# Optimization experiments

Hardware: AMD Instinct MI355X
Metric: run time of the kernel (lower is better)

## Reference

```python
import jax, jax.numpy as jnp
import numpy as np

N_NODES = 32768   # 32 graphs x 1024 points
B_GRAPHS = 32
RATIO = 16
C_IN = 64
HEADS = 4
NEG_SLOPE = 0.2


def setup_inputs() -> dict:
    key = jax.random.key(0)
    ks = jax.random.split(key, 8)
    H, C = HEADS, C_IN
    x = jax.random.normal(ks[0], (N_NODES, C_IN), dtype=jnp.float32)
    edge_index = jax.random.randint(ks[1], (2, 1000), 0, N_NODES)  # ignored by forward
    batch = jnp.repeat(jnp.arange(B_GRAPHS), N_NODES // B_GRAPHS)  # sorted graph ids
    xcent_base = jax.random.normal(ks[2], (RATIO, C_IN), dtype=jnp.float32)
    s = 1.0 / np.sqrt(C_IN)
    W_l = jax.random.normal(ks[3], (C_IN, H * C), dtype=jnp.float32) * s
    b_l = jnp.zeros((H * C,), dtype=jnp.float32)
    W_r = jax.random.normal(ks[4], (C_IN, H * C), dtype=jnp.float32) * s
    b_r = jnp.zeros((H * C,), dtype=jnp.float32)
    att = jax.random.normal(ks[5], (H, C), dtype=jnp.float32) * s
    bias = jnp.zeros((C,), dtype=jnp.float32)
    return {"x": x, "edge_index": edge_index, "batch": batch,
            "xcent_base": xcent_base, "W_l": W_l, "b_l": b_l,
            "W_r": W_r, "b_r": b_r, "att": att, "bias": bias,
            "ratio": RATIO, "batch_size": B_GRAPHS}


def reference(x, edge_index, batch, xcent_base, W_l, b_l, W_r, b_r, att, bias,
              ratio, batch_size):
    # GATv2Conv bipartite: (x_src, x_dst=tiled xcent_base), concat=False (mean over heads)
    H, C = att.shape
    N = x.shape[0]
    T = batch_size * ratio                       # number of target centroids
    # edge list: each source node -> all `ratio` centroids of its graph
    src = jnp.repeat(jnp.arange(N), ratio)       # [E]
    tgt = jnp.tile(jnp.arange(ratio), N) + jnp.repeat(batch, ratio) * ratio  # [E]
    x_dst = jnp.tile(xcent_base, (batch_size, 1))          # [T, C_in]
    x_l = (x @ W_l + b_l).reshape(N, H, C)                 # source transform
    x_r = (x_dst @ W_r + b_r).reshape(T, H, C)             # target transform
    z = x_l[src] + x_r[tgt]                                # [E, H, C]
    z = jnp.where(z >= 0, z, NEG_SLOPE * z)                # LeakyReLU(0.2)
    logit = jnp.einsum('ehc,hc->eh', z, att)               # [E, H]
    # segment softmax over edges sharing a target centroid
    m = jax.ops.segment_max(logit, tgt, num_segments=T)
    ex = jnp.exp(logit - m[tgt])
    den = jax.ops.segment_sum(ex, tgt, num_segments=T)
    alpha = ex / den[tgt]                                  # [E, H]
    out = jax.ops.segment_sum(x_l[src] * alpha[:, :, None], tgt, num_segments=T)
    xcent = out.mean(axis=1) + bias                        # [T, C] (concat=False)
    batchcent = jnp.repeat(jnp.arange(batch_size), ratio)  # [T]
    return xcent, batchcent
```

## Files before the change

### kernel.cpp

```cpp
#include <hip/hip_runtime.h>


typedef __attribute__((ext_vector_type(8))) short short8;
typedef __attribute__((ext_vector_type(4))) float f32x4;

#define NPG 1024
#define NT 512

static __device__ __forceinline__ unsigned short f2bf(float f) {
    unsigned int u = __float_as_uint(f);
    u += 0x7fffu + ((u >> 16) & 1u);
    return (unsigned short)(u >> 16);
}
static __device__ __forceinline__ float bf2f(unsigned short u) {
    return __uint_as_float(((unsigned int)u) << 16);
}

__global__ __launch_bounds__(256) void k0_prep(const float* __restrict__ xcb,
                                               const float* __restrict__ W_l,
                                               const float* __restrict__ W_r,
                                               const float* __restrict__ b_r,
                                               const float* __restrict__ att,
                                               float* __restrict__ xrT,
                                               float* __restrict__ xr_att6,
                                               float* __restrict__ att6,
                                               float* __restrict__ att4,
                                               unsigned short* __restrict__ wt,
                                               float* __restrict__ out) {
    int b = blockIdx.x, t = threadIdx.x;
    if (b < 16) {
        int r = b, hc = t;
        float v = b_r[hc];
#pragma unroll
        for (int k = 0; k < 64; ++k)
            v = fmaf(xcb[r * 64 + k], W_r[k * 256 + hc], v);
        xrT[hc * 16 + r] = v;
        float p = 0.6f * att[hc] * v;
        p += __shfl_xor(p, 1);  p += __shfl_xor(p, 2);
        p += __shfl_xor(p, 4);  p += __shfl_xor(p, 8);
        p += __shfl_xor(p, 16); p += __shfl_xor(p, 32);
        if ((t & 63) == 0) xr_att6[r * 4 + (t >> 6)] = p;
    } else {
        att6[t] = 0.6f * att[t];
        att4[t] = 0.4f * att[t];
        unsigned short tmp[64] __attribute__((aligned(16)));
#pragma unroll
        for (int k = 0; k < 64; ++k) tmp[k] = f2bf(W_l[k * 256 + t]);
#pragma unroll
        for (int q = 0; q < 8; ++q)
            *(short8*)(wt + t * 64 + q * 8) = *(const short8*)(tmp + q * 8);
        out[NT * 64 + t]       = (float)(t >> 4);
        out[NT * 64 + 256 + t] = (float)((256 + t) >> 4);
    }
}

__global__ __launch_bounds__(256, 2) void k1_fused(const float* __restrict__ x,
                                                   const unsigned short* __restrict__ wt,
                                                   const float* __restrict__ b_l,
                                                   const float* __restrict__ att6,
                                                   const float* __restrict__ att4,
                                                   const float* __restrict__ xrT,
                                                   const float* __restrict__ xr_att6,
                                                   unsigned short* __restrict__ ws_pvh,
                                                   float* __restrict__ ws_denp) {
    __shared__ __align__(16) unsigned char smraw[(256 + 64) * 72 * 2];
    unsigned short (*As)[72]  = (unsigned short (*)[72])smraw;
    unsigned short (*xlT)[72] = (unsigned short (*)[72])smraw;
    unsigned short (*exT)[72] = (unsigned short (*)[72])(smraw + 256 * 72 * 2);

    const int t = threadIdx.x;
    const int blk = blockIdx.x;
    const int n0 = blk * 64;

    {
        int n = t >> 2, q = (t & 3) * 16;
        const float* p = x + (size_t)(n0 + n) * 64 + q;
        float4 v0 = *(const float4*)p;
        float4 v1 = *(const float4*)(p + 4);
        float4 v2 = *(const float4*)(p + 8);
        float4 v3 = *(const float4*)(p + 12);
        unsigned short h16[16] __attribute__((aligned(16)));
        h16[0]=f2bf(v0.x); h16[1]=f2bf(v0.y); h16[2]=f2bf(v0.z); h16[3]=f2bf(v0.w);
        h16[4]=f2bf(v1.x); h16[5]=f2bf(v1.y); h16[6]=f2bf(v1.z); h16[7]=f2bf(v1.w);
        h16[8]=f2bf(v2.x); h16[9]=f2bf(v2.y); h16[10]=f2bf(v2.z); h16[11]=f2bf(v2.w);
        h16[12]=f2bf(v3.x); h16[13]=f2bf(v3.y); h16[14]=f2bf(v3.z); h16[15]=f2bf(v3.w);
        *(short8*)(&As[n][q])     = *(const short8*)h16;
        *(short8*)(&As[n][q + 8]) = *(const short8*)(h16 + 8);
    }
    __syncthreads();

    const int l = t & 63;
    const int h = __builtin_amdgcn_readfirstlane(t >> 6);
    const int lm = l & 15, lk = (l >> 4) * 8;

    short8 af[4][2], bfr[4][2];
#pragma unroll
    for (int mt = 0; mt < 4; ++mt)
#pragma unroll
        for (int ks = 0; ks < 2; ++ks)
            af[mt][ks] = *(const short8*)(&As[mt * 16 + lm][ks * 32 + lk]);
#pragma unroll
    for (int nt = 0; nt < 4; ++nt)
#pragma unroll
        for (int ks = 0; ks < 2; ++ks)
            bfr[nt][ks] = *(const short8*)(wt + (size_t)(h * 64 + nt * 16 + lm) * 64 + ks * 32 + lk);

    f32x4 acc[4][4];
#pragma unroll
    for (int mt = 0; mt < 4; ++mt)
#pragma unroll
        for (int nt = 0; nt < 4; ++nt) { f32x4 z = {0.f,0.f,0.f,0.f}; acc[mt][nt] = z; }
#pragma unroll
    for (int mt = 0; mt < 4; ++mt)
#pragma unroll
        for (int nt = 0; nt < 4; ++nt)
#pragma unroll
            for (int ks = 0; ks < 2; ++ks)
                acc[mt][nt] = __builtin_amdgcn_mfma_f32_16x16x32_bf16(
                    af[mt][ks], bfr[nt][ks], acc[mt][nt], 0, 0, 0);

    __syncthreads();

#pragma unroll
    for (int nt = 0; nt < 4; ++nt) {
        float bl = b_l[h * 64 + nt * 16 + lm];
#pragma unroll
        for (int mt = 0; mt < 4; ++mt) {
            unsigned int d0 = (unsigned int)f2bf(acc[mt][nt][0] + bl) |
                              ((unsigned int)f2bf(acc[mt][nt][1] + bl) << 16);
            unsigned int d1 = (unsigned int)f2bf(acc[mt][nt][2] + bl) |
                              ((unsigned int)f2bf(acc[mt][nt][3] + bl) << 16);
            *(uint2*)(&xlT[h * 64 + nt * 16 + lm][mt * 16 + (l >> 4) * 4]) = make_uint2(d0, d1);
        }
    }

    float base = 0.f;
    float lacc[16];
#pragma unroll
    for (int r = 0; r < 16; ++r) lacc[r] = 0.f;
#pragma unroll 8
    for (int c = 0; c < 64; ++c) {
        float xv = bf2f(xlT[h * 64 + c][l]);
        base = fmaf(xv, att6[h * 64 + c], base);
        float a4 = att4[h * 64 + c];
        const float* xp = xrT + (size_t)(h * 64 + c) * 16;
#pragma unroll
        for (int r = 0; r < 16; ++r)
            lacc[r] = fmaf(fabsf(xv + xp[r]), a4, lacc[r]);
    }
#pragma unroll
    for (int r = 0; r < 16; ++r) {
        float ex = __expf(base + lacc[r] + xr_att6[r * 4 + h]);
        exT[h * 16 + r][l] = f2bf(ex);
    }

    short8 ap[2];
#pragma unroll
    for (int ks = 0; ks < 2; ++ks)
        ap[ks] = *(const short8*)(&exT[h * 16 + lm][ks * 32 + lk]);
    short o = (lm == 0) ? (short)0x3F80 : (short)0;
    short8 onesf = {o, o, o, o, o, o, o, o};

    f32x4 pacc[4], dacc;
    { f32x4 z = {0.f,0.f,0.f,0.f}; pacc[0]=z; pacc[1]=z; pacc[2]=z; pacc[3]=z; dacc=z; }
#pragma unroll
    for (int ks = 0; ks < 2; ++ks) {
#pragma unroll
        for (int nt = 0; nt < 4; ++nt) {
            short8 bp = *(const short8*)(&xlT[h * 64 + nt * 16 + lm][ks * 32 + lk]);
            pacc[nt] = __builtin_amdgcn_mfma_f32_16x16x32_bf16(ap[ks], bp, pacc[nt], 0, 0, 0);
        }
        dacc = __builtin_amdgcn_mfma_f32_16x16x32_bf16(ap[ks], onesf, dacc, 0, 0, 0);
    }

    unsigned short* pvb = ws_pvh + ((size_t)blk * 4 + h) * 1024;
#pragma unroll
    for (int nt = 0; nt < 4; ++nt)
#pragma unroll
        for (int j = 0; j < 4; ++j)
            pvb[((l >> 4) * 4 + j) * 64 + nt * 16 + lm] = f2bf(pacc[nt][j]);
    if (lm == 0) {
#pragma unroll
        for (int j = 0; j < 4; ++j)
            ws_denp[((size_t)blk * 4 + h) * 16 + (l >> 4) * 4 + j] = dacc[j];
    }
}

__global__ __launch_bounds__(256) void k2_final(const unsigned short* __restrict__ ws_pvh,
                                                const float* __restrict__ ws_denp,
                                                const float* __restrict__ bias,
                                                float* __restrict__ out) {
    int b = blockIdx.x;
    int g = b >> 2;
    int r = (b & 3) * 4 + (threadIdx.x >> 6);
    int c = threadIdx.x & 63;
    float acc = 0.f;
#pragma unroll
    for (int h = 0; h < 4; ++h) {
        float num = 0.f, den = 0.f;
#pragma unroll
        for (int tl = 0; tl < 16; ++tl) {
            num += bf2f(ws_pvh[(((size_t)(g * 16 + tl)) * 4 + h) * 1024 + r * 64 + c]);
            den += ws_denp[((size_t)(g * 16 + tl) * 4 + h) * 16 + r];
        }
        acc += num / den;
    }
    out[(size_t)(g * 16 + r) * 64 + c] = fmaf(0.25f, acc, bias[c]);
}

extern "C" void kernel_launch(void* const* d_in, const int* in_sizes, int n_in,
                              void* d_out, int out_size, void* d_ws, size_t ws_size,
                              hipStream_t stream) {
    const float* x    = (const float*)d_in[0];
    const float* xcb  = (const float*)d_in[3];
    const float* W_l  = (const float*)d_in[4];
    const float* b_l  = (const float*)d_in[5];
    const float* W_r  = (const float*)d_in[6];
    const float* b_r  = (const float*)d_in[7];
    const float* att  = (const float*)d_in[8];
    const float* bias = (const float*)d_in[9];
    float* out = (float*)d_out;

    unsigned short* ws_pvh = (unsigned short*)d_ws;
    float* ws_denp = (float*)(ws_pvh + 2097152);
    float* xrT     = ws_denp + 32768;
    float* xr_att6 = xrT + 4096;
    float* att6    = xr_att6 + 64;
    float* att4    = att6 + 256;
    unsigned short* wt = (unsigned short*)(att4 + 256);

    k0_prep<<<17, 256, 0, stream>>>(xcb, W_l, W_r, b_r, att, xrT, xr_att6, att6, att4, wt, out);
    k1_fused<<<512, 256, 0, stream>>>(x, wt, b_l, att6, att4, xrT, xr_att6, ws_pvh, ws_denp);
    k2_final<<<128, 256, 0, stream>>>(ws_pvh, ws_denp, bias, out);
}
```

Baseline: 29.93 us.

## Split fused kernel work across 512 threads with XOR-swizzled shared memory

Measured after the change: 32.65 us. 1.09x slower.

```diff
diff --git a/kernel.cpp b/kernel.cpp
--- a/kernel.cpp
+++ b/kernel.cpp
@@ -15,6 +15,7 @@
 static __device__ __forceinline__ float bf2f(unsigned short u) {
     return __uint_as_float(((unsigned int)u) << 16);
 }
+static __device__ __forceinline__ int swz(int row, int unit) { return (unit ^ (row & 7)) << 3; }
 
 __global__ __launch_bounds__(256) void k0_prep(const float* __restrict__ xcb,
                                                const float* __restrict__ W_l,
@@ -54,7 +55,7 @@
     }
 }
 
-__global__ __launch_bounds__(256, 2) void k1_fused(const float* __restrict__ x,
+__global__ __launch_bounds__(512, 4) void k1_fused(const float* __restrict__ x,
                                                    const unsigned short* __restrict__ wt,
                                                    const float* __restrict__ b_l,
                                                    const float* __restrict__ att6,
@@ -63,55 +64,53 @@
                                                    const float* __restrict__ xr_att6,
                                                    unsigned short* __restrict__ ws_pvh,
                                                    float* __restrict__ ws_denp) {
-    __shared__ __align__(16) unsigned char smraw[(256 + 64) * 72 * 2];
-    unsigned short (*As)[72]  = (unsigned short (*)[72])smraw;
-    unsigned short (*xlT)[72] = (unsigned short (*)[72])smraw;
-    unsigned short (*exT)[72] = (unsigned short (*)[72])(smraw + 256 * 72 * 2);
+    __shared__ __align__(16) short LL[320][64];
+    short (*X)[64] = LL;
+    short (*E)[64] = LL + 256;
 
     const int t = threadIdx.x;
     const int blk = blockIdx.x;
     const int n0 = blk * 64;
 
     {
-        int n = t >> 2, q = (t & 3) * 16;
-        const float* p = x + (size_t)(n0 + n) * 64 + q;
+        int n = t >> 3, u = t & 7;
+        const float* p = x + (size_t)(n0 + n) * 64 + u * 8;
         float4 v0 = *(const float4*)p;
         float4 v1 = *(const float4*)(p + 4);
-        float4 v2 = *(const float4*)(p + 8);
-        float4 v3 = *(const float4*)(p + 12);
-        unsigned short h16[16] __attribute__((aligned(16)));
-        h16[0]=f2bf(v0.x); h16[1]=f2bf(v0.y); h16[2]=f2bf(v0.z); h16[3]=f2bf(v0.w);
-        h16[4]=f2bf(v1.x); h16[5]=f2bf(v1.y); h16[6]=f2bf(v1.z); h16[7]=f2bf(v1.w);
-        h16[8]=f2bf(v2.x); h16[9]=f2bf(v2.y); h16[10]=f2bf(v2.z); h16[11]=f2bf(v2.w);
-        h16[12]=f2bf(v3.x); h16[13]=f2bf(v3.y); h16[14]=f2bf(v3.z); h16[15]=f2bf(v3.w);
-        *(short8*)(&As[n][q])     = *(const short8*)h16;
-        *(short8*)(&As[n][q + 8]) = *(const short8*)(h16 + 8);
+        unsigned short h8[8] __attribute__((aligned(16)));
+        h8[0]=f2bf(v0.x); h8[1]=f2bf(v0.y); h8[2]=f2bf(v0.z); h8[3]=f2bf(v0.w);
+        h8[4]=f2bf(v1.x); h8[5]=f2bf(v1.y); h8[6]=f2bf(v1.z); h8[7]=f2bf(v1.w);
+        *(short8*)(&X[n][swz(n, u)]) = *(const short8*)h8;
     }
     __syncthreads();
 
     const int l = t & 63;
-    const int h = __builtin_amdgcn_readfirstlane(t >> 6);
-    const int lm = l & 15, lk = (l >> 4) * 8;
-
-    short8 af[4][2], bfr[4][2];
-#pragma unroll
-    for (int mt = 0; mt < 4; ++mt)
+    const int w = t >> 6;
+    const int h    = __builtin_amdgcn_readfirstlane(w & 3);
+    const int half = __builtin_amdgcn_readfirstlane(w >> 2);
+    const int lm = l & 15, lq = l >> 4;
+
+    short8 af[2][2], bfr[4][2];
+#pragma unroll
+    for (int mt = 0; mt < 2; ++mt)
+#pragma unroll
+        for (int ks = 0; ks < 2; ++ks) {
+            int row = half * 32 + mt * 16 + lm;
+            af[mt][ks] = *(const short8*)(&X[row][swz(row, ks * 4 + lq)]);
+        }
+#pragma unroll
+    for (int nt = 0; nt < 4; ++nt)
 #pragma unroll
         for (int ks = 0; ks < 2; ++ks)
-            af[mt][ks] = *(const short8*)(&As[mt * 16 + lm][ks * 32 + lk]);
-#pragma unroll
-    for (int nt = 0; nt < 4; ++nt)
-#pragma unroll
-        for (int ks = 0; ks < 2; ++ks)
-            bfr[nt][ks] = *(const short8*)(wt + (size_t)(h * 64 + nt * 16 + lm) * 64 + ks * 32 + lk);
-
-    f32x4 acc[4][4];
-#pragma unroll
-    for (int mt = 0; mt < 4; ++mt)
+            bfr[nt][ks] = *(const short8*)(wt + (size_t)(h * 64 + nt * 16 + lm) * 64 + ks * 32 + lq * 8);
+
+    f32x4 acc[2][4];
+#pragma unroll
+    for (int mt = 0; mt < 2; ++mt)
 #pragma unroll
         for (int nt = 0; nt < 4; ++nt) { f32x4 z = {0.f,0.f,0.f,0.f}; acc[mt][nt] = z; }
 #pragma unroll
-    for (int mt = 0; mt < 4; ++mt)
+    for (int mt = 0; mt < 2; ++mt)
 #pragma unroll
         for (int nt = 0; nt < 4; ++nt)
 #pragma unroll
@@ -125,64 +124,76 @@
     for (int nt = 0; nt < 4; ++nt) {
         float bl = b_l[h * 64 + nt * 16 + lm];
 #pragma unroll
-        for (int mt = 0; mt < 4; ++mt) {
+        for (int mt = 0; mt < 2; ++mt) {
             unsigned int d0 = (unsigned int)f2bf(acc[mt][nt][0] + bl) |
                               ((unsigned int)f2bf(acc[mt][nt][1] + bl) << 16);
             unsigned int d1 = (unsigned int)f2bf(acc[mt][nt][2] + bl) |
                               ((unsigned int)f2bf(acc[mt][nt][3] + bl) << 16);
-            *(uint2*)(&xlT[h * 64 + nt * 16 + lm][mt * 16 + (l >> 4) * 4]) = make_uint2(d0, d1);
-        }
-    }
+            int row = h * 64 + nt * 16 + lm;
+            int ncol = half * 32 + mt * 16 + lq * 4;
+            int col = swz(row, ncol >> 3) + (ncol & 7);
+            *(uint2*)(&X[row][col]) = make_uint2(d0, d1);
+        }
+    }
+    __syncthreads();
 
     float base = 0.f;
-    float lacc[16];
-#pragma unroll
-    for (int r = 0; r < 16; ++r) lacc[r] = 0.f;
-#pragma unroll 8
+    float lacc[8];
+#pragma unroll
+    for (int rr = 0; rr < 8; ++rr) lacc[rr] = 0.f;
+#pragma unroll 4
     for (int c = 0; c < 64; ++c) {
-        float xv = bf2f(xlT[h * 64 + c][l]);
-        base = fmaf(xv, att6[h * 64 + c], base);
-        float a4 = att4[h * 64 + c];
-        const float* xp = xrT + (size_t)(h * 64 + c) * 16;
-#pragma unroll
-        for (int r = 0; r < 16; ++r)
-            lacc[r] = fmaf(fabsf(xv + xp[r]), a4, lacc[r]);
-    }
-#pragma unroll
-    for (int r = 0; r < 16; ++r) {
-        float ex = __expf(base + lacc[r] + xr_att6[r * 4 + h]);
-        exT[h * 16 + r][l] = f2bf(ex);
-    }
+        int row = h * 64 + c;
+        float xv = bf2f((unsigned short)X[row][swz(row, l >> 3) + (l & 7)]);
+        base = fmaf(xv, att6[row], base);
+        float a4 = att4[row];
+        const float* xp = xrT + (size_t)row * 16 + half * 8;
+#pragma unroll
+        for (int rr = 0; rr < 8; ++rr)
+            lacc[rr] = fmaf(fabsf(xv + xp[rr]), a4, lacc[rr]);
+    }
+#pragma unroll
+    for (int rr = 0; rr < 8; ++rr) {
+        int r = half * 8 + rr;
+        float ex = __expf(base + lacc[rr] + xr_att6[r * 4 + h]);
+        int erow = h * 16 + r;
+        E[erow][swz(erow, l >> 3) + (l & 7)] = (short)f2bf(ex);
+    }
+    __syncthreads();
 
     short8 ap[2];
 #pragma unroll
-    for (int ks = 0; ks < 2; ++ks)
-        ap[ks] = *(const short8*)(&exT[h * 16 + lm][ks * 32 + lk]);
-    short o = (lm == 0) ? (short)0x3F80 : (short)0;
-    short8 onesf = {o, o, o, o, o, o, o, o};
-
-    f32x4 pacc[4], dacc;
-    { f32x4 z = {0.f,0.f,0.f,0.f}; pacc[0]=z; pacc[1]=z; pacc[2]=z; pacc[3]=z; dacc=z; }
-#pragma unroll
     for (int ks = 0; ks < 2; ++ks) {
-#pragma unroll
-        for (int nt = 0; nt < 4; ++nt) {
-            short8 bp = *(const short8*)(&xlT[h * 64 + nt * 16 + lm][ks * 32 + lk]);
-            pacc[nt] = __builtin_amdgcn_mfma_f32_16x16x32_bf16(ap[ks], bp, pacc[nt], 0, 0, 0);
-        }
-        dacc = __builtin_amdgcn_mfma_f32_16x16x32_bf16(ap[ks], onesf, dacc, 0, 0, 0);
+        int erow = h * 16 + lm;
+        ap[ks] = *(const short8*)(&E[erow][swz(erow, ks * 4 + lq)]);
+    }
+    f32x4 pacc[2], dacc;
+    { f32x4 z = {0.f,0.f,0.f,0.f}; pacc[0]=z; pacc[1]=z; dacc=z; }
+#pragma unroll
+    for (int ks = 0; ks < 2; ++ks) {
+#pragma unroll
+        for (int ntl = 0; ntl < 2; ++ntl) {
+            int row = h * 64 + (half * 2 + ntl) * 16 + lm;
+            short8 bp = *(const short8*)(&X[row][swz(row, ks * 4 + lq)]);
+            pacc[ntl] = __builtin_amdgcn_mfma_f32_16x16x32_bf16(ap[ks], bp, pacc[ntl], 0, 0, 0);
+        }
+        if (half == 0) {
+            short o = (lm == 0) ? (short)0x3F80 : (short)0;
+            short8 onesf = {o, o, o, o, o, o, o, o};
+            dacc = __builtin_amdgcn_mfma_f32_16x16x32_bf16(ap[ks], onesf, dacc, 0, 0, 0);
+        }
     }
 
     unsigned short* pvb = ws_pvh + ((size_t)blk * 4 + h) * 1024;
 #pragma unroll
-    for (int nt = 0; nt < 4; ++nt)
+    for (int ntl = 0; ntl < 2; ++ntl)
 #pragma unroll
         for (int j = 0; j < 4; ++j)
-            pvb[((l >> 4) * 4 + j) * 64 + nt * 16 + lm] = f2bf(pacc[nt][j]);
-    if (lm == 0) {
+            pvb[(lq * 4 + j) * 64 + (half * 2 + ntl) * 16 + lm] = f2bf(pacc[ntl][j]);
+    if (half == 0 && lm == 0) {
 #pragma unroll
         for (int j = 0; j < 4; ++j)
-            ws_denp[((size_t)blk * 4 + h) * 16 + (l >> 4) * 4 + j] = dacc[j];
+            ws_denp[((size_t)blk * 4 + h) * 16 + lq * 4 + j] = dacc[j];
     }
 }
 
@@ -230,6 +241,6 @@
     unsigned short* wt = (unsigned short*)(att4 + 256);
 
     k0_prep<<<17, 256, 0, stream>>>(xcb, W_l, W_r, b_r, att, xrT, xr_att6, att6, att4, wt, out);
-    k1_fused<<<512, 256, 0, stream>>>(x, wt, b_l, att6, att4, xrT, xr_att6, ws_pvh, ws_denp);
+    k1_fused<<<512, 512, 0, stream>>>(x, wt, b_l, att6, att4, xrT, xr_att6, ws_pvh, ws_denp);
     k2_final<<<128, 256, 0, stream>>>(ws_pvh, ws_denp, bias, out);
 }
```
